# Kernel optimization log

Hardware: AMD Instinct MI355X
Metric: run time of the kernel (lower is better)

## Reference

```python
import jax, jax.numpy as jnp
import numpy as np

N_NODES = 40000
N_EDGES = 640000
IN_CH = 128
HID_CH = 256
EDGE_DIM = 64
N_SAMP = 2048
T = 1.0
EPS_GIN = 0.0
EPS_NORM = 1e-12


def setup_inputs() -> dict:
    key = jax.random.key(0)
    ks = jax.random.split(key, 12)
    x = jax.random.normal(ks[0], (N_NODES, IN_CH), dtype=jnp.float32)
    edge_index = jax.random.randint(ks[1], (2, N_EDGES), 0, N_NODES, dtype=jnp.int64)
    edge_attr = jax.random.normal(ks[2], (N_EDGES, EDGE_DIM), dtype=jnp.float32)
    pos_ind = jax.random.randint(ks[3], (N_SAMP,), 0, N_NODES, dtype=jnp.int64)
    neg_ind = jax.random.randint(ks[4], (N_SAMP,), 0, N_NODES, dtype=jnp.int64)
    # GINEConv internal edge projection Linear(64 -> 128)
    We = jax.random.normal(ks[5], (EDGE_DIM, IN_CH), dtype=jnp.float32) / np.sqrt(EDGE_DIM)
    be = jnp.zeros((IN_CH,), dtype=jnp.float32)
    # MLP: Linear(128->256), ReLU, Linear(256->256)
    W1 = jax.random.normal(ks[6], (IN_CH, HID_CH), dtype=jnp.float32) / np.sqrt(IN_CH)
    b1 = jnp.zeros((HID_CH,), dtype=jnp.float32)
    W2 = jax.random.normal(ks[7], (HID_CH, HID_CH), dtype=jnp.float32) / np.sqrt(HID_CH)
    b2 = jnp.zeros((HID_CH,), dtype=jnp.float32)
    thresholding_node = jax.random.normal(ks[8], (1, HID_CH), dtype=jnp.float32)
    return {"x": x, "edge_index": edge_index, "edge_attr": edge_attr,
            "pos_ind": pos_ind, "neg_ind": neg_ind,
            "We": We, "be": be, "W1": W1, "b1": b1, "W2": W2, "b2": b2,
            "thresholding_node": thresholding_node}


def _normalize(v):
    n = jnp.linalg.norm(v, axis=-1, keepdims=True)
    return v / jnp.maximum(n, EPS_NORM)


def reference(x, edge_index, edge_attr, pos_ind, neg_ind,
              We, be, W1, b1, W2, b2, thresholding_node):
    src, dst = edge_index[0], edge_index[1]  # PyG: message from x_j (src) to target i (dst)
    edge_emb = edge_attr @ We + be                    # [E, in_ch]
    msg = jax.nn.relu(x[src] + edge_emb)              # gather + add + relu
    agg = jax.ops.segment_sum(msg, dst, num_segments=x.shape[0])  # scatter-add
    h = (1.0 + EPS_GIN) * x + agg
    emb = jax.nn.relu(h @ W1 + b1) @ W2 + b2          # [N, hid]

    center = _normalize(emb[0])                       # [hid]
    pos = _normalize(emb[pos_ind])                    # [P, hid]
    neg = _normalize(emb[neg_ind])                    # [Q, hid]
    thr = _normalize(thresholding_node)               # [1, hid]

    pos_score_mean = (center[None, :] * pos).sum(-1).mean(-1)
    neg_score_mean = (center[None, :] * neg).sum(-1).mean(-1)
    thr_score = (center * thr).sum(-1)                # [1]

    pos_loss = jnp.log(jnp.clip(jax.nn.sigmoid((pos_score_mean - thr_score) / T), 1e-12)).mean()
    neg_loss = jnp.log(jnp.clip(jax.nn.sigmoid((thr_score - neg_score_mean) / T), 1e-12)).mean()
    return -pos_loss - neg_loss
```

## Files before the change

### kernel.cpp

```cpp
#include <hip/hip_runtime.h>
#include <math.h>

#define N_NODES 40000
#define N_EDGES 640000
#define IN_CH 128
#define HID_CH 256
#define EDGE_DIM 64
#define N_SAMP 2048
#define NSEL (1 + 2 * N_SAMP)
#define MAXU 4097
#define QCAP 512

__global__ __launch_bounds__(256) void init_kernel(
    int* __restrict__ slot, int* __restrict__ counters, float4* __restrict__ agg4)
{
    const int i = blockIdx.x * 256 + threadIdx.x;
    const int n = gridDim.x * 256;
    for (int j = i; j < 40960; j += n) slot[j] = -1;
    if (i < 32) counters[i] = 0;
    const float4 z = make_float4(0.f, 0.f, 0.f, 0.f);
    for (int j = i; j < (MAXU * IN_CH) / 4; j += n) agg4[j] = z;
}

__global__ __launch_bounds__(256) void flag_kernel(
    const int* __restrict__ pos, const int* __restrict__ neg,
    int* __restrict__ slot, int* __restrict__ counters)
{
    int r = blockIdx.x * 256 + threadIdx.x;
    if (r >= NSEL) return;
    int node = (r == 0) ? 0 : (r <= N_SAMP ? pos[r - 1] : neg[r - 1 - N_SAMP]);
    int old = atomicCAS(&slot[node], -1, -2);
    if (old == -1) slot[node] = atomicAdd(&counters[1], 1);
}

struct EdgeSmem {
    float sWe[EDGE_DIM * IN_CH];
    float sAttr[4][16 * EDGE_DIM];
    int qE[QCAP], qL[QCAP];
    int sE[4][16], sS[4][16], sL[4][16];
    int sWc[4], sQbase, sHead, sTail;
};

__device__ __forceinline__ void process_tile(
    EdgeSmem* es, int base, int rem,
    const float* __restrict__ x, const int* __restrict__ ei,
    const float* __restrict__ edge_attr, float be0, float be1,
    float* __restrict__ agg_c, int wave, int lane)
{
    if (lane < 16) {
        int p = wave * 16 + lane;
        bool v = p < rem;
        int qi = (base + p) & (QCAP - 1);
        int e = v ? es->qE[qi] : 0;
        es->sE[wave][lane] = e;
        es->sS[wave][lane] = v ? ei[e] : 0;
        es->sL[wave][lane] = v ? es->qL[qi] : -1;
    }
    __syncthreads();
    {
        int sub = lane >> 4, q = lane & 15;
#pragma unroll
        for (int p = 0; p < 4; ++p) {
            int j = p * 4 + sub;
            int e = es->sE[wave][j];
            ((float4*)&es->sAttr[wave][j * EDGE_DIM])[q] =
                ((const float4*)(edge_attr + (size_t)e * EDGE_DIM))[q];
        }
    }
    __syncthreads();

    float acc0[16], acc1[16];
#pragma unroll
    for (int j = 0; j < 16; ++j) { acc0[j] = 0.f; acc1[j] = 0.f; }
    for (int k0 = 0; k0 < EDGE_DIM; k0 += 4) {
        float w0[4], w1[4];
#pragma unroll
        for (int kk = 0; kk < 4; ++kk) {
            w0[kk] = es->sWe[(k0 + kk) * IN_CH + lane];
            w1[kk] = es->sWe[(k0 + kk) * IN_CH + 64 + lane];
        }
#pragma unroll
        for (int j = 0; j < 16; ++j) {
            float4 a = *(const float4*)&es->sAttr[wave][j * EDGE_DIM + k0];
            acc0[j] += a.x * w0[0] + a.y * w0[1] + a.z * w0[2] + a.w * w0[3];
            acc1[j] += a.x * w1[0] + a.y * w1[1] + a.z * w1[2] + a.w * w1[3];
        }
    }
#pragma unroll
    for (int j = 0; j < 16; ++j) {
        int sl = es->sL[wave][j];
        if (sl >= 0) {
            int s = es->sS[wave][j];
            float m0 = fmaxf(x[(size_t)s * IN_CH + lane] + acc0[j] + be0, 0.f);
            float m1 = fmaxf(x[(size_t)s * IN_CH + 64 + lane] + acc1[j] + be1, 0.f);
            atomicAdd(&agg_c[(size_t)sl * IN_CH + lane], m0);
            atomicAdd(&agg_c[(size_t)sl * IN_CH + 64 + lane], m1);
        }
    }
}

__global__ __launch_bounds__(256) void edge_kernel(
    const float* __restrict__ x, const int* __restrict__ ei,
    const float* __restrict__ edge_attr, const float* __restrict__ We,
    const float* __restrict__ be, const int* __restrict__ slot,
    float* __restrict__ agg_c)
{
    __shared__ EdgeSmem es;
    const int tid = threadIdx.x, wave = tid >> 6, lane = tid & 63;

    {
        const float4* s4 = (const float4*)We;
        float4* d4 = (float4*)es.sWe;
        for (int i = tid; i < (EDGE_DIM * IN_CH) / 4; i += 256) d4[i] = s4[i];
    }
    if (tid == 0) { es.sHead = 0; es.sTail = 0; }
    __syncthreads();
    const float be0 = be[lane], be1 = be[64 + lane];

    const int base0 = blockIdx.x * 1024;
#pragma unroll 1
    for (int c = 0; c < 4; ++c) {
        int e = base0 + c * 256 + tid;
        int d = ei[N_EDGES + e];
        int sl = slot[d];
        bool valid = (sl >= 0);
        unsigned long long m = __ballot(valid);
        int wrank = __popcll(m & ((1ULL << lane) - 1ULL));
        if (lane == 0) es.sWc[wave] = __popcll(m);
        __syncthreads();
        if (tid == 0) {
            int t = 0;
            for (int i = 0; i < 4; ++i) { int cc = es.sWc[i]; es.sWc[i] = t; t += cc; }
            es.sQbase = es.sTail;
            es.sTail = es.sQbase + t;
        }
        __syncthreads();
        if (valid) {
            int idx = (es.sQbase + es.sWc[wave] + wrank) & (QCAP - 1);
            es.qE[idx] = e;
            es.qL[idx] = sl;
        }
        while (true) {
            __syncthreads();
            int h = es.sHead, t = es.sTail;
            if (t - h < 64) break;
            process_tile(&es, h, 64, x, ei, edge_attr, be0, be1, agg_c, wave, lane);
            if (tid == 0) es.sHead = h + 64;
        }
    }
    __syncthreads();
    int h = es.sHead, t = es.sTail;
    if (t - h > 0)
        process_tile(&es, h, t - h, x, ei, edge_attr, be0, be1, agg_c, wave, lane);
}

struct MlpSmem {
    float sin_[17][IN_CH];
    float shid[17][HID_CH];
    float semb[17][HID_CH];
    int snode[17], sslot[17];
    float wpos[4], wneg[4];
};

__global__ __launch_bounds__(256) void mlpscore_kernel(
    const float* __restrict__ x, const float* __restrict__ agg_c,
    const int* __restrict__ slot, const int* __restrict__ pos,
    const int* __restrict__ neg, const float* __restrict__ W1,
    const float* __restrict__ b1, const float* __restrict__ W2,
    const float* __restrict__ b2, float* __restrict__ fsum,
    float* __restrict__ embC)
{
    __shared__ MlpSmem ms;
    const int tid = threadIdx.x, wave = tid >> 6, lane = tid & 63;
    const int r0 = blockIdx.x * 16;
    if (tid < 17) {
        int node = 0;
        if (tid < 16) {
            int r = r0 + tid;
            if (r < NSEL && r > 0)
                node = (r <= N_SAMP) ? pos[r - 1] : neg[r - 1 - N_SAMP];
        }
        ms.snode[tid] = node;
        ms.sslot[tid] = slot[node];
    }
    __syncthreads();
    for (int i = tid; i < 17 * (IN_CH / 4); i += 256) {
        int rr = i / 32, k4 = i % 32;
        int n = ms.snode[rr], sl = ms.sslot[rr];
        float4 xa = ((const float4*)(x + (size_t)n * IN_CH))[k4];
        float4 ga = ((const float4*)(agg_c + (size_t)sl * IN_CH))[k4];
        ((float4*)ms.sin_[rr])[k4] =
            make_float4(xa.x + ga.x, xa.y + ga.y, xa.z + ga.z, xa.w + ga.w);
    }
    __syncthreads();

    float acc[17];
#pragma unroll
    for (int rr = 0; rr < 17; ++rr) acc[rr] = 0.f;
    for (int k0 = 0; k0 < IN_CH; k0 += 4) {
        float w[4];
#pragma unroll
        for (int kk = 0; kk < 4; ++kk) w[kk] = W1[(k0 + kk) * HID_CH + tid];
#pragma unroll
        for (int rr = 0; rr < 17; ++rr) {
            float4 h = *(const float4*)&ms.sin_[rr][k0];
            acc[rr] += h.x * w[0] + h.y * w[1] + h.z * w[2] + h.w * w[3];
        }
    }
    float bb1 = b1[tid];
#pragma unroll
    for (int rr = 0; rr < 17; ++rr) ms.shid[rr][tid] = fmaxf(acc[rr] + bb1, 0.f);
    __syncthreads();

#pragma unroll
    for (int rr = 0; rr < 17; ++rr) acc[rr] = 0.f;
    for (int k0 = 0; k0 < HID_CH; k0 += 4) {
        float w[4];
#pragma unroll
        for (int kk = 0; kk < 4; ++kk) w[kk] = W2[(k0 + kk) * HID_CH + tid];
#pragma unroll
        for (int rr = 0; rr < 17; ++rr) {
            float4 h = *(const float4*)&ms.shid[rr][k0];
            acc[rr] += h.x * w[0] + h.y * w[1] + h.z * w[2] + h.w * w[3];
        }
    }
    float bb2 = b2[tid];
#pragma unroll
    for (int rr = 0; rr < 17; ++rr) ms.semb[rr][tid] = acc[rr] + bb2;
    __syncthreads();

    const float4 c4 = ((const float4*)ms.semb[16])[lane];
    float css = c4.x * c4.x + c4.y * c4.y + c4.z * c4.z + c4.w * c4.w;
#pragma unroll
    for (int off = 32; off; off >>= 1) css += __shfl_xor(css, off, 64);
    const float cn = fmaxf(sqrtf(css), 1e-12f);

    float psum = 0.f, nsum = 0.f;
    for (int rr = wave; rr < 16; rr += 4) {
        int r = r0 + rr;
        if (r < 1 || r >= NSEL) continue;
        const float4 v = ((const float4*)ms.semb[rr])[lane];
        float vv = v.x * v.x + v.y * v.y + v.z * v.z + v.w * v.w;
        float cv = c4.x * v.x + c4.y * v.y + c4.z * v.z + c4.w * v.w;
#pragma unroll
        for (int off = 32; off; off >>= 1) {
            vv += __shfl_xor(vv, off, 64);
            cv += __shfl_xor(cv, off, 64);
        }
        float score = cv / (cn * fmaxf(sqrtf(vv), 1e-12f));
        if (r <= N_SAMP) psum += score; else nsum += score;
    }
    if (lane == 0) { ms.wpos[wave] = psum; ms.wneg[wave] = nsum; }
    __syncthreads();
    if (tid == 0) {
        atomicAdd(&fsum[0], ms.wpos[0] + ms.wpos[1] + ms.wpos[2] + ms.wpos[3]);
        atomicAdd(&fsum[1], ms.wneg[0] + ms.wneg[1] + ms.wneg[2] + ms.wneg[3]);
    }
    if (blockIdx.x == 0) embC[tid] = ms.semb[16][tid];
}

__global__ __launch_bounds__(256) void loss_kernel(
    const float* __restrict__ embC, const float* __restrict__ thrn,
    const float* __restrict__ fsum, float* __restrict__ out)
{
    __shared__ float rcc[4], rtt[4], rct[4];
    const int tid = threadIdx.x, wave = tid >> 6, lane = tid & 63;
    float c = embC[tid], t = thrn[tid];
    float cc = c * c, tt = t * t, ct = c * t;
#pragma unroll
    for (int off = 32; off; off >>= 1) {
        cc += __shfl_xor(cc, off, 64);
        tt += __shfl_xor(tt, off, 64);
        ct += __shfl_xor(ct, off, 64);
    }
    if (lane == 0) { rcc[wave] = cc; rtt[wave] = tt; rct[wave] = ct; }
    __syncthreads();
    if (tid == 0) {
        float scc = rcc[0] + rcc[1] + rcc[2] + rcc[3];
        float stt = rtt[0] + rtt[1] + rtt[2] + rtt[3];
        float sct = rct[0] + rct[1] + rct[2] + rct[3];
        float thr = sct / (fmaxf(sqrtf(scc), 1e-12f) * fmaxf(sqrtf(stt), 1e-12f));
        float pm = fsum[0] / (float)N_SAMP;
        float nm = fsum[1] / (float)N_SAMP;
        float s1 = 1.f / (1.f + expf(-(pm - thr)));
        float s2 = 1.f / (1.f + expf(-(thr - nm)));
        s1 = fmaxf(s1, 1e-12f);
        s2 = fmaxf(s2, 1e-12f);
        out[0] = -(logf(s1) + logf(s2));
    }
}

extern "C" void kernel_launch(void* const* d_in, const int* in_sizes, int n_in,
                              void* d_out, int out_size, void* d_ws, size_t ws_size,
                              hipStream_t stream)
{
    const float* x         = (const float*)d_in[0];
    const int*   ei        = (const int*)d_in[1];
    const float* edge_attr = (const float*)d_in[2];
    const int*   pos       = (const int*)d_in[3];
    const int*   neg       = (const int*)d_in[4];
    const float* We        = (const float*)d_in[5];
    const float* be        = (const float*)d_in[6];
    const float* W1        = (const float*)d_in[7];
    const float* b1        = (const float*)d_in[8];
    const float* W2        = (const float*)d_in[9];
    const float* b2        = (const float*)d_in[10];
    const float* thrn      = (const float*)d_in[11];
    float* out = (float*)d_out;

    int* slot     = (int*)d_ws;
    int* counters = slot + 40960;
    float* fsum   = (float*)(counters + 2);
    float* agg_c  = (float*)(counters + 32);
    float* embC   = agg_c + 524800;

    init_kernel<<<256, 256, 0, stream>>>(slot, counters, (float4*)agg_c);
    flag_kernel<<<(NSEL + 255) / 256, 256, 0, stream>>>(pos, neg, slot, counters);
    edge_kernel<<<N_EDGES / 1024, 256, 0, stream>>>(x, ei, edge_attr, We, be, slot, agg_c);
    mlpscore_kernel<<<(NSEL + 15) / 16, 256, 0, stream>>>(
        x, agg_c, slot, pos, neg, W1, b1, W2, b2, fsum, embC);
    loss_kernel<<<1, 256, 0, stream>>>(embC, thrn, fsum, out);
}
```

Before: 400.4 us.

## Replace atomic edge scatter with counting-sort by destination and per-node reduction

Edges targeting selected nodes are counting-sorted by destination slot via histogram, single-block scan, and atomic scatter into a packed (edge, src) list. The edge kernel then assigns one wave per selected node, accumulating messages in registers and writing aggregates directly, removing float atomics, the shared queue with its barriers, and the aggregate zeroing. It costs three extra kernel launches, a second pass over the destination indices, and partially filled 16-edge tiles for low-degree nodes.

Result: faster. 380.5 us (-5.0%).

```diff
diff --git a/kernel.cpp b/kernel.cpp
--- a/kernel.cpp
+++ b/kernel.cpp
@@ -9,17 +9,15 @@
 #define N_SAMP 2048
 #define NSEL (1 + 2 * N_SAMP)
 #define MAXU 4097
-#define QCAP 512
+#define EGRID 768
 
 __global__ __launch_bounds__(256) void init_kernel(
-    int* __restrict__ slot, int* __restrict__ counters, float4* __restrict__ agg4)
+    int* __restrict__ slot, int* __restrict__ counters, int* __restrict__ hist)
 {
     const int i = blockIdx.x * 256 + threadIdx.x;
-    const int n = gridDim.x * 256;
-    for (int j = i; j < 40960; j += n) slot[j] = -1;
+    slot[i] = -1;
     if (i < 32) counters[i] = 0;
-    const float4 z = make_float4(0.f, 0.f, 0.f, 0.f);
-    for (int j = i; j < (MAXU * IN_CH) / 4; j += n) agg4[j] = z;
+    if (i < 5120) hist[i] = 0;
 }
 
 __global__ __launch_bounds__(256) void flag_kernel(
@@ -33,125 +31,117 @@
     if (old == -1) slot[node] = atomicAdd(&counters[1], 1);
 }
 
-struct EdgeSmem {
-    float sWe[EDGE_DIM * IN_CH];
-    float sAttr[4][16 * EDGE_DIM];
-    int qE[QCAP], qL[QCAP];
-    int sE[4][16], sS[4][16], sL[4][16];
-    int sWc[4], sQbase, sHead, sTail;
-};
-
-__device__ __forceinline__ void process_tile(
-    EdgeSmem* es, int base, int rem,
-    const float* __restrict__ x, const int* __restrict__ ei,
-    const float* __restrict__ edge_attr, float be0, float be1,
-    float* __restrict__ agg_c, int wave, int lane)
-{
-    if (lane < 16) {
-        int p = wave * 16 + lane;
-        bool v = p < rem;
-        int qi = (base + p) & (QCAP - 1);
-        int e = v ? es->qE[qi] : 0;
-        es->sE[wave][lane] = e;
-        es->sS[wave][lane] = v ? ei[e] : 0;
-        es->sL[wave][lane] = v ? es->qL[qi] : -1;
-    }
-    __syncthreads();
-    {
-        int sub = lane >> 4, q = lane & 15;
-#pragma unroll
-        for (int p = 0; p < 4; ++p) {
-            int j = p * 4 + sub;
-            int e = es->sE[wave][j];
-            ((float4*)&es->sAttr[wave][j * EDGE_DIM])[q] =
-                ((const float4*)(edge_attr + (size_t)e * EDGE_DIM))[q];
-        }
-    }
-    __syncthreads();
-
-    float acc0[16], acc1[16];
-#pragma unroll
-    for (int j = 0; j < 16; ++j) { acc0[j] = 0.f; acc1[j] = 0.f; }
-    for (int k0 = 0; k0 < EDGE_DIM; k0 += 4) {
-        float w0[4], w1[4];
-#pragma unroll
-        for (int kk = 0; kk < 4; ++kk) {
-            w0[kk] = es->sWe[(k0 + kk) * IN_CH + lane];
-            w1[kk] = es->sWe[(k0 + kk) * IN_CH + 64 + lane];
-        }
-#pragma unroll
-        for (int j = 0; j < 16; ++j) {
-            float4 a = *(const float4*)&es->sAttr[wave][j * EDGE_DIM + k0];
-            acc0[j] += a.x * w0[0] + a.y * w0[1] + a.z * w0[2] + a.w * w0[3];
-            acc1[j] += a.x * w1[0] + a.y * w1[1] + a.z * w1[2] + a.w * w1[3];
-        }
-    }
-#pragma unroll
-    for (int j = 0; j < 16; ++j) {
-        int sl = es->sL[wave][j];
-        if (sl >= 0) {
-            int s = es->sS[wave][j];
-            float m0 = fmaxf(x[(size_t)s * IN_CH + lane] + acc0[j] + be0, 0.f);
-            float m1 = fmaxf(x[(size_t)s * IN_CH + 64 + lane] + acc1[j] + be1, 0.f);
-            atomicAdd(&agg_c[(size_t)sl * IN_CH + lane], m0);
-            atomicAdd(&agg_c[(size_t)sl * IN_CH + 64 + lane], m1);
-        }
+__global__ __launch_bounds__(256) void hist_kernel(
+    const int* __restrict__ ei, const int* __restrict__ slot,
+    int* __restrict__ hist)
+{
+    int e = blockIdx.x * 256 + threadIdx.x;
+    int sl = slot[ei[N_EDGES + e]];
+    if (sl >= 0) atomicAdd(&hist[sl], 1);
+}
+
+__global__ __launch_bounds__(1024) void scan_kernel(
+    const int* __restrict__ hist, int* __restrict__ cursor,
+    int* __restrict__ start)
+{
+    __shared__ int tmp[1024];
+    const int t = threadIdx.x;
+    int v[5]; int s = 0;
+#pragma unroll
+    for (int i = 0; i < 5; ++i) { v[i] = hist[t * 5 + i]; s += v[i]; }
+    tmp[t] = s;
+    __syncthreads();
+    for (int d = 1; d < 1024; d <<= 1) {
+        int a = (t >= d) ? tmp[t - d] : 0;
+        __syncthreads();
+        tmp[t] += a;
+        __syncthreads();
+    }
+    int run = tmp[t] - s;
+#pragma unroll
+    for (int i = 0; i < 5; ++i) {
+        cursor[t * 5 + i] = run;
+        start[t * 5 + i] = run;
+        run += v[i];
+    }
+}
+
+__global__ __launch_bounds__(256) void scatter_kernel(
+    const int* __restrict__ ei, const int* __restrict__ slot,
+    int* __restrict__ cursor, int2* __restrict__ sorted2)
+{
+    int e = blockIdx.x * 256 + threadIdx.x;
+    int sl = slot[ei[N_EDGES + e]];
+    if (sl >= 0) {
+        int p = atomicAdd(&cursor[sl], 1);
+        sorted2[p] = make_int2(e, ei[e]);
     }
 }
 
 __global__ __launch_bounds__(256) void edge_kernel(
-    const float* __restrict__ x, const int* __restrict__ ei,
-    const float* __restrict__ edge_attr, const float* __restrict__ We,
-    const float* __restrict__ be, const int* __restrict__ slot,
-    float* __restrict__ agg_c)
-{
-    __shared__ EdgeSmem es;
+    const float* __restrict__ x, const float* __restrict__ edge_attr,
+    const float* __restrict__ We, const float* __restrict__ be,
+    const int* __restrict__ counters, const int* __restrict__ start,
+    const int2* __restrict__ sorted2, float* __restrict__ agg_c)
+{
+    __shared__ float sWe[EDGE_DIM * IN_CH];
+    __shared__ float sAttr[4][16 * EDGE_DIM];
     const int tid = threadIdx.x, wave = tid >> 6, lane = tid & 63;
+    const int U = counters[1];
 
     {
         const float4* s4 = (const float4*)We;
-        float4* d4 = (float4*)es.sWe;
+        float4* d4 = (float4*)sWe;
         for (int i = tid; i < (EDGE_DIM * IN_CH) / 4; i += 256) d4[i] = s4[i];
     }
-    if (tid == 0) { es.sHead = 0; es.sTail = 0; }
     __syncthreads();
     const float be0 = be[lane], be1 = be[64 + lane];
-
-    const int base0 = blockIdx.x * 1024;
-#pragma unroll 1
-    for (int c = 0; c < 4; ++c) {
-        int e = base0 + c * 256 + tid;
-        int d = ei[N_EDGES + e];
-        int sl = slot[d];
-        bool valid = (sl >= 0);
-        unsigned long long m = __ballot(valid);
-        int wrank = __popcll(m & ((1ULL << lane) - 1ULL));
-        if (lane == 0) es.sWc[wave] = __popcll(m);
-        __syncthreads();
-        if (tid == 0) {
-            int t = 0;
-            for (int i = 0; i < 4; ++i) { int cc = es.sWc[i]; es.sWc[i] = t; t += cc; }
-            es.sQbase = es.sTail;
-            es.sTail = es.sQbase + t;
-        }
-        __syncthreads();
-        if (valid) {
-            int idx = (es.sQbase + es.sWc[wave] + wrank) & (QCAP - 1);
-            es.qE[idx] = e;
-            es.qL[idx] = sl;
-        }
-        while (true) {
-            __syncthreads();
-            int h = es.sHead, t = es.sTail;
-            if (t - h < 64) break;
-            process_tile(&es, h, 64, x, ei, edge_attr, be0, be1, agg_c, wave, lane);
-            if (tid == 0) es.sHead = h + 64;
-        }
-    }
-    __syncthreads();
-    int h = es.sHead, t = es.sTail;
-    if (t - h > 0)
-        process_tile(&es, h, t - h, x, ei, edge_attr, be0, be1, agg_c, wave, lane);
+    const int sub = lane >> 4, q = lane & 15;
+
+    for (int s = blockIdx.x * 4 + wave; s < U; s += EGRID * 4) {
+        const int st = start[s], en = start[s + 1];
+        float r0 = 0.f, r1 = 0.f;
+        for (int t = st; t < en; t += 16) {
+            const int cnt = min(16, en - t);
+            int2 v = make_int2(0, 0);
+            if (lane < cnt) v = sorted2[t + lane];
+            const int ev = v.x, sv = v.y;
+#pragma unroll
+            for (int p = 0; p < 4; ++p) {
+                int j = p * 4 + sub;
+                int e = __shfl(ev, j);
+                if (j < cnt)
+                    ((float4*)&sAttr[wave][j * EDGE_DIM])[q] =
+                        ((const float4*)(edge_attr + (size_t)e * EDGE_DIM))[q];
+            }
+            float acc0[16], acc1[16];
+#pragma unroll
+            for (int j = 0; j < 16; ++j) { acc0[j] = 0.f; acc1[j] = 0.f; }
+            for (int k0 = 0; k0 < EDGE_DIM; k0 += 4) {
+                float w0[4], w1[4];
+#pragma unroll
+                for (int kk = 0; kk < 4; ++kk) {
+                    w0[kk] = sWe[(k0 + kk) * IN_CH + lane];
+                    w1[kk] = sWe[(k0 + kk) * IN_CH + 64 + lane];
+                }
+#pragma unroll
+                for (int j = 0; j < 16; ++j) {
+                    float4 a = *(const float4*)&sAttr[wave][j * EDGE_DIM + k0];
+                    acc0[j] += a.x * w0[0] + a.y * w0[1] + a.z * w0[2] + a.w * w0[3];
+                    acc1[j] += a.x * w1[0] + a.y * w1[1] + a.z * w1[2] + a.w * w1[3];
+                }
+            }
+#pragma unroll
+            for (int j = 0; j < 16; ++j) {
+                if (j >= cnt) break;
+                int s2 = __shfl(sv, j);
+                r0 += fmaxf(x[(size_t)s2 * IN_CH + lane] + acc0[j] + be0, 0.f);
+                r1 += fmaxf(x[(size_t)s2 * IN_CH + 64 + lane] + acc1[j] + be1, 0.f);
+            }
+        }
+        agg_c[(size_t)s * IN_CH + lane] = r0;
+        agg_c[(size_t)s * IN_CH + 64 + lane] = r1;
+    }
 }
 
 struct MlpSmem {
@@ -311,12 +301,20 @@
     int* slot     = (int*)d_ws;
     int* counters = slot + 40960;
     float* fsum   = (float*)(counters + 2);
-    float* agg_c  = (float*)(counters + 32);
+    int* hist     = counters + 32;
+    int* cursor   = hist + 5120;
+    int* start    = cursor + 5120;
+    int2* sorted2 = (int2*)(start + 5120);
+    float* agg_c  = (float*)(sorted2 + N_EDGES);
     float* embC   = agg_c + 524800;
 
-    init_kernel<<<256, 256, 0, stream>>>(slot, counters, (float4*)agg_c);
+    init_kernel<<<160, 256, 0, stream>>>(slot, counters, hist);
     flag_kernel<<<(NSEL + 255) / 256, 256, 0, stream>>>(pos, neg, slot, counters);
-    edge_kernel<<<N_EDGES / 1024, 256, 0, stream>>>(x, ei, edge_attr, We, be, slot, agg_c);
+    hist_kernel<<<N_EDGES / 256, 256, 0, stream>>>(ei, slot, hist);
+    scan_kernel<<<1, 1024, 0, stream>>>(hist, cursor, start);
+    scatter_kernel<<<N_EDGES / 256, 256, 0, stream>>>(ei, slot, cursor, sorted2);
+    edge_kernel<<<EGRID, 256, 0, stream>>>(x, edge_attr, We, be, counters,
+                                           start, sorted2, agg_c);
     mlpscore_kernel<<<(NSEL + 15) / 16, 256, 0, stream>>>(
         x, agg_c, slot, pos, neg, W1, b1, W2, b2, fsum, embC);
     loss_kernel<<<1, 256, 0, stream>>>(embC, thrn, fsum, out);
```
